# Performance work log

Hardware: AMD Instinct MI355X
Metric: run time of the kernel (lower is better)

The kernel has to match this reference:

```python
import jax, jax.numpy as jnp
import numpy as np

D_MODEL = 1024
NUM_HEADS = 16
HEAD_DIM = D_MODEL // NUM_HEADS
EPS = 1e-06


def setup_inputs() -> dict:
    key = jax.random.key(0)
    ks = jax.random.split(key, 7)
    B, T, D = 4, 4096, D_MODEL
    scale = 1.0 / np.sqrt(D)
    x = jax.random.normal(ks[0], (B, T, D), dtype=jnp.float32)
    Wq = jax.random.normal(ks[1], (D, D), dtype=jnp.float32) * scale
    Wk = jax.random.normal(ks[2], (D, D), dtype=jnp.float32) * scale
    Wv = jax.random.normal(ks[3], (D, D), dtype=jnp.float32) * scale
    Wo = jax.random.normal(ks[4], (D, D), dtype=jnp.float32) * scale
    Wg = jax.random.normal(ks[5], (D, D), dtype=jnp.float32) * scale
    bg = jnp.zeros((D,), dtype=jnp.float32)
    return {"x": x, "Wq": Wq, "Wk": Wk, "Wv": Wv, "Wo": Wo, "Wg": Wg, "bg": bg}


def phi(x):
    return jax.nn.elu(x) + 1.0


def reference(x, Wq, Wk, Wv, Wo, Wg, bg):
    B, T, D = x.shape
    H, Hd = NUM_HEADS, HEAD_DIM
    # torch nn.Linear: y = x @ W.T
    q = phi((x @ Wq.T).reshape(B, T, H, Hd))
    k = phi((x @ Wk.T).reshape(B, T, H, Hd))
    v = (x @ Wv.T).reshape(B, T, H, Hd)
    k_sum = k.sum(axis=1)                              # [B,H,Hd]
    kv_sum = jnp.einsum('bthd,bthd->bhd', k, v)        # [B,H,Hd] (elementwise-product reduction, as in source)
    # out[b,t,h,v] = sum_d q[b,t,h,d]*kv_sum[b,h,d], identical for every v
    s = jnp.einsum('bthd,bhd->bth', q, kv_sum)         # [B,T,H]
    z = jnp.einsum('bthd,bhd->bth', q, k_sum) + EPS    # [B,T,H]
    out = (s / z)[..., None] * jnp.ones((Hd,), dtype=x.dtype)  # broadcast over head_dim
    out = out.reshape(B, T, D)
    gate = jax.nn.sigmoid(x @ Wg.T + bg)
    return gate * out + (1.0 - gate) * x
```

## Files before the change

kernel.cpp:

```cpp
#include <hip/hip_runtime.h>

#define D_MODEL 1024
#define TSEQ    4096
#define BATCH   4
#define MROWS   (BATCH * TSEQ)
#define KDIM    1024
#define NDIM    1024
#define EPSV    1e-6f

typedef __attribute__((ext_vector_type(8))) short short8;
typedef __attribute__((ext_vector_type(4))) float floatx4;

__device__ inline unsigned short f2bf(float f) {
  unsigned u = __float_as_uint(f);
  unsigned r = (u + 0x7FFFu + ((u >> 16) & 1u)) >> 16;
  return (unsigned short)r;
}
__device__ inline float bf2f(unsigned short h) {
  return __uint_as_float(((unsigned)h) << 16);
}
__device__ inline float phi_f(float x) { return x > 0.f ? x + 1.f : __expf(x); }

#define NX4 4194304
#define NW4 262144
#define NZ4 2048

__global__ __launch_bounds__(256) void prep_kernel(
    const float* __restrict__ x,  const float* __restrict__ wq,
    const float* __restrict__ wk, const float* __restrict__ wv,
    const float* __restrict__ wg,
    unsigned short* __restrict__ xb,  unsigned short* __restrict__ wqb,
    unsigned short* __restrict__ wkb, unsigned short* __restrict__ wvb,
    unsigned short* __restrict__ wgb, float* __restrict__ zbase)
{
  long i = (long)blockIdx.x * 256 + threadIdx.x;
  const float* src; unsigned short* dst; long j = i;
  if (j < NX4) { src = x; dst = xb; }
  else {
    j -= NX4;
    if (j < NW4) { src = wq; dst = wqb; }
    else { j -= NW4;
      if (j < NW4) { src = wk; dst = wkb; }
      else { j -= NW4;
        if (j < NW4) { src = wv; dst = wvb; }
        else { j -= NW4;
          if (j < NW4) { src = wg; dst = wgb; }
          else { j -= NW4;
            if (j < NZ4) { float4 zz = {0.f,0.f,0.f,0.f}; ((float4*)zbase)[j] = zz; }
            return;
          }
        }
      }
    }
  }
  float4 f = ((const float4*)src)[j];
  ushort4 o;
  o.x = f2bf(f.x); o.y = f2bf(f.y); o.z = f2bf(f.z); o.w = f2bf(f.w);
  ((ushort4*)dst)[j] = o;
}

#define BM 128
#define BN 128
#define BK 32

__global__ __launch_bounds__(256, 2) void gemm_kv_kernel(
    const unsigned short* __restrict__ A,
    const unsigned short* __restrict__ Wk, const unsigned short* __restrict__ Wv,
    float* __restrict__ ksum, float* __restrict__ kvsum)
{
  const int bn = blockIdx.x;
  const int bm = blockIdx.y;

  __shared__ __align__(16) unsigned short As[BM * BK];
  __shared__ __align__(16) unsigned short Bk[BN * BK];
  __shared__ __align__(16) unsigned short Bv[BN * BK];

  const int tid  = threadIdx.x;
  const int lane = tid & 63;
  const int w    = tid >> 6;
  const int wr   = (w >> 1) * 64;
  const int wc   = (w & 1) * 64;

  floatx4 ak[4][4], av[4][4];
#pragma unroll
  for (int i = 0; i < 4; i++)
#pragma unroll
    for (int j = 0; j < 4; j++) {
      floatx4 zz = {0.f,0.f,0.f,0.f}; ak[i][j] = zz; av[i][j] = zz;
    }

  const unsigned short* Ablk  = A  + (size_t)bm * BM * KDIM;
  const unsigned short* Bkblk = Wk + (size_t)bn * BN * KDIM;
  const unsigned short* Bvblk = Wv + (size_t)bn * BN * KDIM;

  const int la = lane & 15;
  const int lk = (lane >> 4) * 8;

  for (int kt = 0; kt < KDIM; kt += BK) {
    __syncthreads();
#pragma unroll
    for (int c = 0; c < 2; c++) {
      int f   = tid + c * 256;
      int row = f >> 2;
      int col = (f & 3) * 8;
      size_t goff = (size_t)row * KDIM + kt + col;
      __builtin_amdgcn_global_load_lds(
          (const __attribute__((address_space(1))) void*)(Ablk + goff),
          (__attribute__((address_space(3))) void*)(As + (size_t)f * 8), 16, 0, 0);
      __builtin_amdgcn_global_load_lds(
          (const __attribute__((address_space(1))) void*)(Bkblk + goff),
          (__attribute__((address_space(3))) void*)(Bk + (size_t)f * 8), 16, 0, 0);
      __builtin_amdgcn_global_load_lds(
          (const __attribute__((address_space(1))) void*)(Bvblk + goff),
          (__attribute__((address_space(3))) void*)(Bv + (size_t)f * 8), 16, 0, 0);
    }
    __syncthreads();

    short8 af[4], bk[4], bv[4];
#pragma unroll
    for (int i = 0; i < 4; i++) {
      af[i] = *(const short8*)&As[(wr + i * 16 + la) * BK + lk];
      bk[i] = *(const short8*)&Bk[(wc + i * 16 + la) * BK + lk];
      bv[i] = *(const short8*)&Bv[(wc + i * 16 + la) * BK + lk];
    }
#pragma unroll
    for (int i = 0; i < 4; i++)
#pragma unroll
      for (int j = 0; j < 4; j++) {
        ak[i][j] = __builtin_amdgcn_mfma_f32_16x16x32_bf16(af[i], bk[j], ak[i][j], 0, 0, 0);
        av[i][j] = __builtin_amdgcn_mfma_f32_16x16x32_bf16(af[i], bv[j], av[i][j], 0, 0, 0);
      }
  }

  const int b = bm >> 5;
  float kp[4] = {0.f,0.f,0.f,0.f};
  float vp[4] = {0.f,0.f,0.f,0.f};
#pragma unroll
  for (int j = 0; j < 4; j++)
#pragma unroll
    for (int i = 0; i < 4; i++)
#pragma unroll
      for (int r = 0; r < 4; r++) {
        float kk = phi_f(ak[i][j][r]);
        kp[j] += kk;
        vp[j] += kk * av[i][j][r];
      }
#pragma unroll
  for (int j = 0; j < 4; j++) {
    kp[j] += __shfl_xor(kp[j], 16, 64); kp[j] += __shfl_xor(kp[j], 32, 64);
    vp[j] += __shfl_xor(vp[j], 16, 64); vp[j] += __shfl_xor(vp[j], 32, 64);
  }
  if (lane < 16) {
#pragma unroll
    for (int j = 0; j < 4; j++) {
      int col = bn * BN + wc + j * 16 + lane;
      atomicAdd(ksum  + (size_t)b * D_MODEL + col, kp[j]);
      atomicAdd(kvsum + (size_t)b * D_MODEL + col, vp[j]);
    }
  }
}

__global__ __launch_bounds__(512) void gemm_qg_kernel(
    const unsigned short* __restrict__ A,
    const unsigned short* __restrict__ Wq, const unsigned short* __restrict__ Wg,
    const float* __restrict__ x, const float* __restrict__ bg,
    const float* __restrict__ ksum, const float* __restrict__ kvsum,
    float* __restrict__ out)
{
  const int bn = blockIdx.x;
  const int bm = blockIdx.y;

  __shared__ __align__(16) unsigned short As[BM * BK];
  __shared__ __align__(16) unsigned short Bq[BN * BK];
  __shared__ __align__(16) unsigned short Bg[BN * BK];
  __shared__ float o_lds[2 * BM];

  const int tid  = threadIdx.x;
  const int lane = tid & 63;
  const int w    = tid >> 6;
  const int is_g = w >> 2;
  const int wl   = w & 3;
  const int wr   = (wl >> 1) * 64;
  const int wc   = (wl & 1) * 64;

  floatx4 acc[4][4];
#pragma unroll
  for (int i = 0; i < 4; i++)
#pragma unroll
    for (int j = 0; j < 4; j++) { floatx4 zz = {0.f,0.f,0.f,0.f}; acc[i][j] = zz; }

  const unsigned short* Ablk  = A + (size_t)bm * BM * KDIM;
  const unsigned short* Bqblk = Wq + (size_t)bn * BN * KDIM;
  const unsigned short* Bgblk = Wg + (size_t)bn * BN * KDIM;

  const int la = lane & 15;
  const int lk = (lane >> 4) * 8;
  const unsigned short* Bsm = is_g ? Bg : Bq;

  for (int kt = 0; kt < KDIM; kt += BK) {
    __syncthreads();
    {
      int f   = tid;
      int row = f >> 2;
      int col = (f & 3) * 8;
      size_t goff = (size_t)row * KDIM + kt + col;
      __builtin_amdgcn_global_load_lds(
          (const __attribute__((address_space(1))) void*)(Ablk + goff),
          (__attribute__((address_space(3))) void*)(As + (size_t)f * 8), 16, 0, 0);
      __builtin_amdgcn_global_load_lds(
          (const __attribute__((address_space(1))) void*)(Bqblk + goff),
          (__attribute__((address_space(3))) void*)(Bq + (size_t)f * 8), 16, 0, 0);
      __builtin_amdgcn_global_load_lds(
          (const __attribute__((address_space(1))) void*)(Bgblk + goff),
          (__attribute__((address_space(3))) void*)(Bg + (size_t)f * 8), 16, 0, 0);
    }
    __syncthreads();

    short8 af[4], bfg[4];
#pragma unroll
    for (int i = 0; i < 4; i++) {
      af[i]  = *(const short8*)&As[(wr + i * 16 + la) * BK + lk];
      bfg[i] = *(const short8*)&Bsm[(wc + i * 16 + la) * BK + lk];
    }
#pragma unroll
    for (int i = 0; i < 4; i++)
#pragma unroll
      for (int j = 0; j < 4; j++)
        acc[i][j] = __builtin_amdgcn_mfma_f32_16x16x32_bf16(af[i], bfg[j], acc[i][j], 0, 0, 0);
  }

  const int b  = bm >> 5;
  const int ro = (lane >> 4) * 4;
  const int co = lane & 15;
  const int hl = wc >> 6;

  if (!is_g) {
    float kvv[4], ksv[4];
#pragma unroll
    for (int j = 0; j < 4; j++) {
      int col = bn * BN + wc + j * 16 + co;
      kvv[j] = kvsum[(size_t)b * D_MODEL + col];
      ksv[j] = ksum [(size_t)b * D_MODEL + col];
    }
#pragma unroll
    for (int i = 0; i < 4; i++)
#pragma unroll
      for (int r = 0; r < 4; r++) {
        float s = 0.f, z = 0.f;
#pragma unroll
        for (int j = 0; j < 4; j++) {
          float qq = phi_f(acc[i][j][r]);
          s += qq * kvv[j]; z += qq * ksv[j];
        }
#pragma unroll
        for (int m = 1; m < 16; m <<= 1) {
          s += __shfl_xor(s, m, 64);
          z += __shfl_xor(z, m, 64);
        }
        if (co == 0) o_lds[hl * BM + wr + i * 16 + ro + r] = s / (z + EPSV);
      }
  }
  __syncthreads();
  if (is_g) {
    float bgv[4];
#pragma unroll
    for (int j = 0; j < 4; j++) bgv[j] = bg[bn * BN + wc + j * 16 + co];
#pragma unroll
    for (int i = 0; i < 4; i++)
#pragma unroll
      for (int r = 0; r < 4; r++) {
        int rowl = wr + i * 16 + ro + r;
        int grow = bm * BM + rowl;
        float ov = o_lds[hl * BM + rowl];
#pragma unroll
        for (int j = 0; j < 4; j++) {
          int gcol = bn * BN + wc + j * 16 + co;
          float gt = 1.f / (1.f + __expf(-(acc[i][j][r] + bgv[j])));
          float xv = x[(size_t)grow * D_MODEL + gcol];
          out[(size_t)grow * D_MODEL + gcol] = gt * ov + (1.f - gt) * xv;
        }
      }
  }
}

extern "C" void kernel_launch(void* const* d_in, const int* in_sizes, int n_in,
                              void* d_out, int out_size, void* d_ws, size_t ws_size,
                              hipStream_t stream) {
  (void)in_sizes; (void)n_in; (void)out_size; (void)ws_size;
  const float* x  = (const float*)d_in[0];
  const float* Wq = (const float*)d_in[1];
  const float* Wk = (const float*)d_in[2];
  const float* Wv = (const float*)d_in[3];
  const float* Wg = (const float*)d_in[5];
  const float* bg = (const float*)d_in[6];
  float* out = (float*)d_out;

  char* ws = (char*)d_ws;
  const size_t xel = (size_t)MROWS * D_MODEL;
  const size_t wel = (size_t)NDIM * KDIM;
  unsigned short* xbf = (unsigned short*)ws; ws += xel * 2;
  unsigned short* wqb = (unsigned short*)ws; ws += wel * 2;
  unsigned short* wkb = (unsigned short*)ws; ws += wel * 2;
  unsigned short* wvb = (unsigned short*)ws; ws += wel * 2;
  unsigned short* wgb = (unsigned short*)ws; ws += wel * 2;
  float* ksum  = (float*)ws; ws += (size_t)BATCH * D_MODEL * 4;
  float* kvsum = (float*)ws; ws += (size_t)BATCH * D_MODEL * 4;

  const long total4 = (long)NX4 + 4L * NW4 + NZ4;
  prep_kernel<<<(int)((total4 + 255) / 256), 256, 0, stream>>>(
      x, Wq, Wk, Wv, Wg, xbf, wqb, wkb, wvb, wgb, ksum);

  dim3 g1(NDIM / BN, MROWS / BM);
  gemm_kv_kernel<<<g1, 256, 0, stream>>>(xbf, wkb, wvb, ksum, kvsum);

  dim3 g2(NDIM / BN, MROWS / BM);
  gemm_qg_kernel<<<g2, 512, 0, stream>>>(xbf, wqb, wgb, x, bg, ksum, kvsum, out);
}
```

Measured before the change: 296.4 us.

## Double K-tile depth to 64 and XOR-swizzle LDS layout in both GEMM kernels

Raises BK from 32 to 64 so each K iteration loads twice as much into LDS and runs two MFMA sub-steps per barrier pair, halving the number of __syncthreads rounds. The LDS tiles are stored with an XOR swizzle of the 16-byte chunk index by row, and the fragment reads use the matching swizzle to avoid bank conflicts. The larger tiles double LDS use. The kv kernel also drops its min-blocks-per-SM launch bound, which may lower occupancy or change register allocation.

```diff
diff --git a/kernel.cpp b/kernel.cpp
--- a/kernel.cpp
+++ b/kernel.cpp
@@ -61,9 +61,10 @@
 
 #define BM 128
 #define BN 128
-#define BK 32
-
-__global__ __launch_bounds__(256, 2) void gemm_kv_kernel(
+#define BK 64
+
+
+__global__ __launch_bounds__(256) void gemm_kv_kernel(
     const unsigned short* __restrict__ A,
     const unsigned short* __restrict__ Wk, const unsigned short* __restrict__ Wv,
     float* __restrict__ ksum, float* __restrict__ kvsum)
@@ -93,43 +94,48 @@
   const unsigned short* Bkblk = Wk + (size_t)bn * BN * KDIM;
   const unsigned short* Bvblk = Wv + (size_t)bn * BN * KDIM;
 
-  const int la = lane & 15;
-  const int lk = (lane >> 4) * 8;
+  const int la  = lane & 15;
+  const int lg  = lane >> 4;
+  const int lx  = lane & 7;
 
   for (int kt = 0; kt < KDIM; kt += BK) {
     __syncthreads();
 #pragma unroll
-    for (int c = 0; c < 2; c++) {
-      int f   = tid + c * 256;
-      int row = f >> 2;
-      int col = (f & 3) * 8;
-      size_t goff = (size_t)row * KDIM + kt + col;
+    for (int c = 0; c < 4; c++) {
+      int s   = tid + c * 256;
+      int r   = s >> 3;
+      int gc  = (s & 7) ^ (r & 7);
+      size_t goff = (size_t)r * KDIM + kt + gc * 8;
       __builtin_amdgcn_global_load_lds(
           (const __attribute__((address_space(1))) void*)(Ablk + goff),
-          (__attribute__((address_space(3))) void*)(As + (size_t)f * 8), 16, 0, 0);
+          (__attribute__((address_space(3))) void*)(As + (size_t)s * 8), 16, 0, 0);
       __builtin_amdgcn_global_load_lds(
           (const __attribute__((address_space(1))) void*)(Bkblk + goff),
-          (__attribute__((address_space(3))) void*)(Bk + (size_t)f * 8), 16, 0, 0);
+          (__attribute__((address_space(3))) void*)(Bk + (size_t)s * 8), 16, 0, 0);
       __builtin_amdgcn_global_load_lds(
           (const __attribute__((address_space(1))) void*)(Bvblk + goff),
-          (__attribute__((address_space(3))) void*)(Bv + (size_t)f * 8), 16, 0, 0);
+          (__attribute__((address_space(3))) void*)(Bv + (size_t)s * 8), 16, 0, 0);
     }
     __syncthreads();
 
-    short8 af[4], bk[4], bv[4];
-#pragma unroll
-    for (int i = 0; i < 4; i++) {
-      af[i] = *(const short8*)&As[(wr + i * 16 + la) * BK + lk];
-      bk[i] = *(const short8*)&Bk[(wc + i * 16 + la) * BK + lk];
-      bv[i] = *(const short8*)&Bv[(wc + i * 16 + la) * BK + lk];
-    }
-#pragma unroll
-    for (int i = 0; i < 4; i++)
-#pragma unroll
-      for (int j = 0; j < 4; j++) {
-        ak[i][j] = __builtin_amdgcn_mfma_f32_16x16x32_bf16(af[i], bk[j], ak[i][j], 0, 0, 0);
-        av[i][j] = __builtin_amdgcn_mfma_f32_16x16x32_bf16(af[i], bv[j], av[i][j], 0, 0, 0);
-      }
+#pragma unroll
+    for (int ks = 0; ks < 2; ks++) {
+      const int gx = ((ks * 4 + lg) ^ lx);
+      short8 af[4], bk[4], bv[4];
+#pragma unroll
+      for (int i = 0; i < 4; i++) {
+        af[i] = *(const short8*)&As[((wr + i * 16 + la) * 8 + gx) * 8];
+        bk[i] = *(const short8*)&Bk[((wc + i * 16 + la) * 8 + gx) * 8];
+        bv[i] = *(const short8*)&Bv[((wc + i * 16 + la) * 8 + gx) * 8];
+      }
+#pragma unroll
+      for (int i = 0; i < 4; i++)
+#pragma unroll
+        for (int j = 0; j < 4; j++) {
+          ak[i][j] = __builtin_amdgcn_mfma_f32_16x16x32_bf16(af[i], bk[j], ak[i][j], 0, 0, 0);
+          av[i][j] = __builtin_amdgcn_mfma_f32_16x16x32_bf16(af[i], bv[j], av[i][j], 0, 0, 0);
+        }
+    }
   }
 
   const int b = bm >> 5;
@@ -194,39 +200,45 @@
   const unsigned short* Bgblk = Wg + (size_t)bn * BN * KDIM;
 
   const int la = lane & 15;
-  const int lk = (lane >> 4) * 8;
+  const int lg = lane >> 4;
+  const int lx = lane & 7;
   const unsigned short* Bsm = is_g ? Bg : Bq;
 
   for (int kt = 0; kt < KDIM; kt += BK) {
     __syncthreads();
-    {
-      int f   = tid;
-      int row = f >> 2;
-      int col = (f & 3) * 8;
-      size_t goff = (size_t)row * KDIM + kt + col;
+#pragma unroll
+    for (int c = 0; c < 2; c++) {
+      int s   = tid + c * 512;
+      int r   = s >> 3;
+      int gc  = (s & 7) ^ (r & 7);
+      size_t goff = (size_t)r * KDIM + kt + gc * 8;
       __builtin_amdgcn_global_load_lds(
           (const __attribute__((address_space(1))) void*)(Ablk + goff),
-          (__attribute__((address_space(3))) void*)(As + (size_t)f * 8), 16, 0, 0);
+          (__attribute__((address_space(3))) void*)(As + (size_t)s * 8), 16, 0, 0);
       __builtin_amdgcn_global_load_lds(
           (const __attribute__((address_space(1))) void*)(Bqblk + goff),
-          (__attribute__((address_space(3))) void*)(Bq + (size_t)f * 8), 16, 0, 0);
+          (__attribute__((address_space(3))) void*)(Bq + (size_t)s * 8), 16, 0, 0);
       __builtin_amdgcn_global_load_lds(
           (const __attribute__((address_space(1))) void*)(Bgblk + goff),
-          (__attribute__((address_space(3))) void*)(Bg + (size_t)f * 8), 16, 0, 0);
+          (__attribute__((address_space(3))) void*)(Bg + (size_t)s * 8), 16, 0, 0);
     }
     __syncthreads();
 
-    short8 af[4], bfg[4];
-#pragma unroll
-    for (int i = 0; i < 4; i++) {
-      af[i]  = *(const short8*)&As[(wr + i * 16 + la) * BK + lk];
-      bfg[i] = *(const short8*)&Bsm[(wc + i * 16 + la) * BK + lk];
-    }
-#pragma unroll
-    for (int i = 0; i < 4; i++)
-#pragma unroll
-      for (int j = 0; j < 4; j++)
-        acc[i][j] = __builtin_amdgcn_mfma_f32_16x16x32_bf16(af[i], bfg[j], acc[i][j], 0, 0, 0);
+#pragma unroll
+    for (int ks = 0; ks < 2; ks++) {
+      const int gx = ((ks * 4 + lg) ^ lx);
+      short8 af[4], bfg[4];
+#pragma unroll
+      for (int i = 0; i < 4; i++) {
+        af[i]  = *(const short8*)&As[((wr + i * 16 + la) * 8 + gx) * 8];
+        bfg[i] = *(const short8*)&Bsm[((wc + i * 16 + la) * 8 + gx) * 8];
+      }
+#pragma unroll
+      for (int i = 0; i < 4; i++)
+#pragma unroll
+        for (int j = 0; j < 4; j++)
+          acc[i][j] = __builtin_amdgcn_mfma_f32_16x16x32_bf16(af[i], bfg[j], acc[i][j], 0, 0, 0);
+    }
   }
 
   const int b  = bm >> 5;
```

Result: slower. 326.1 us (+10.0%).
